# Kernel tuning notes

Measured on AMD Instinct MI355X. Metric: run time of the kernel, lower is better.

Reference implementation:

```python
import jax, jax.numpy as jnp
import numpy as np

PRE, POST, BATCH, HIST = 2048, 2048, 64, 50
CONN_PROB = 0.1


def setup_inputs() -> dict:
    key = jax.random.key(0)
    k1, k2, k3, k4 = jax.random.split(key, 4)
    pre_spikes = jax.random.uniform(k1, (BATCH, PRE), dtype=jnp.float32)
    post_spikes = jax.random.uniform(k2, (BATCH, POST), dtype=jnp.float32)
    connectivity_mask = (jax.random.uniform(k3, (PRE, POST)) < CONN_PROB).astype(jnp.float32)
    synaptic_weights = jax.random.normal(k4, (PRE, POST), dtype=jnp.float32) * 0.1 * connectivity_mask
    return {
        "pre_spikes": pre_spikes,
        "post_spikes": post_spikes,
        "current_time": 0,  # <= 1.0 -> plasticity (formation/pruning) branch skipped, as in warm-up
        "synaptic_weights": synaptic_weights,
        "connectivity_mask": connectivity_mask,
        "pre_activity": jnp.zeros((PRE,), jnp.float32),
        "post_activity": jnp.zeros((POST,), jnp.float32),
        "correlation_history": jnp.zeros((PRE, POST, HIST), jnp.float32),
        "connection_lifetimes": jnp.zeros((PRE, POST), jnp.float32),
        "correlation_index": 7,  # static rolling-buffer write position
    }


def reference(pre_spikes, post_spikes, current_time, synaptic_weights,
              connectivity_mask, pre_activity, post_activity,
              correlation_history, connection_lifetimes, correlation_index):
    # EMA activity traces
    pre_mean = pre_spikes.mean(axis=0)    # [PRE]
    post_mean = post_spikes.mean(axis=0)  # [POST]
    new_pre_activity = 0.99 * pre_activity + 0.01 * pre_mean
    new_post_activity = 0.99 * post_activity + 0.01 * post_mean

    # scatter outer-product correlation into rolling history buffer
    idx = correlation_index % HIST
    current_correlation = jnp.outer(pre_mean, post_mean)              # [PRE, POST]
    new_history = correlation_history.at[:, :, idx].set(current_correlation)

    # masked weight matmul
    effective_weights = synaptic_weights * connectivity_mask          # [PRE, POST]
    synaptic_current = pre_spikes @ effective_weights                 # [BATCH, POST]

    # connection lifetime accumulation
    new_lifetimes = connection_lifetimes + connectivity_mask

    avg_correlation = new_history.mean(axis=-1)                       # [PRE, POST]
    return (synaptic_current, new_pre_activity, new_post_activity,
            new_history, new_lifetimes, avg_correlation)
```

## Files before the change

### kernel.cpp

```cpp
#include <hip/hip_runtime.h>

#define PRE   2048
#define POST  2048
#define BATCH 64
#define HIST  50

#define OFF_SYN      0
#define OFF_PRE_ACT  131072
#define OFF_POST_ACT 133120
#define OFF_HIST     135168
#define OFF_LIFE     209850368
#define OFF_AVG      214044672

__global__ __launch_bounds__(256) void k_means(
    const float* __restrict__ pre, const float* __restrict__ post,
    const float* __restrict__ pre_act, const float* __restrict__ post_act,
    float* __restrict__ out, float* __restrict__ ws_means) {
  const int t = blockIdx.x * 256 + threadIdx.x;

  float4* outz = reinterpret_cast<float4*>(out + OFF_SYN);
  const float4 z = make_float4(0.f, 0.f, 0.f, 0.f);
#pragma unroll
  for (int i = 0; i < 8; ++i) outz[t + i * 4096] = z;

  if (t < PRE) {
    float s = 0.f;
#pragma unroll 8
    for (int b = 0; b < BATCH; ++b) s += pre[b * PRE + t];
    const float m = s * (1.0f / BATCH);
    ws_means[t] = m;
    out[OFF_PRE_ACT + t] = 0.99f * pre_act[t] + 0.01f * m;
  } else {
    const int c = t - PRE;
    float s = 0.f;
#pragma unroll 8
    for (int b = 0; b < BATCH; ++b) s += post[b * POST + c];
    const float m = s * (1.0f / BATCH);
    ws_means[PRE + c] = m;
    out[OFF_POST_ACT + c] = 0.99f * post_act[c] + 0.01f * m;
  }
}

__global__ __launch_bounds__(256) void k_matmul(
    const float* __restrict__ pre, const float* __restrict__ W,
    const float* __restrict__ M, float* __restrict__ out) {
  __shared__ float ew[64 * 256];

  const int jt = blockIdx.x & 7;
  const int ks = blockIdx.x >> 3;
  const int j0 = jt * 256;
  const int k0 = ks * 64;
  const int t = threadIdx.x;

#pragma unroll
  for (int it = 0; it < 16; ++it) {
    const int lin = (t + it * 256) * 4;
    const int kk = lin >> 8;
    const int jj = lin & 255;
    const float4 w4 = *reinterpret_cast<const float4*>(&W[(k0 + kk) * POST + j0 + jj]);
    const float4 m4 = *reinterpret_cast<const float4*>(&M[(k0 + kk) * POST + j0 + jj]);
    float4 e;
    e.x = w4.x * m4.x; e.y = w4.y * m4.y; e.z = w4.z * m4.z; e.w = w4.w * m4.w;
    *reinterpret_cast<float4*>(&ew[kk * 256 + jj]) = e;
  }
  __syncthreads();

  const int tj = t & 31;
  const int tb = t >> 5;
  const int jb = tj * 8;
  const int bb0 = tb * 8;

  float acc[8][8];
#pragma unroll
  for (int r = 0; r < 8; ++r)
#pragma unroll
    for (int c = 0; c < 8; ++c) acc[r][c] = 0.f;

  const float4* ew4 = reinterpret_cast<const float4*>(ew);

  for (int kk4 = 0; kk4 < 16; ++kk4) {
    float4 pr[8];
#pragma unroll
    for (int r = 0; r < 8; ++r)
      pr[r] = *reinterpret_cast<const float4*>(&pre[(bb0 + r) * PRE + k0 + kk4 * 4]);
#pragma unroll
    for (int e = 0; e < 4; ++e) {
      const int kk = kk4 * 4 + e;
      const float4 e0 = ew4[kk * 64 + tj * 2];
      const float4 e1 = ew4[kk * 64 + tj * 2 + 1];
#pragma unroll
      for (int r = 0; r < 8; ++r) {
        const float pv = (e == 0) ? pr[r].x : (e == 1) ? pr[r].y : (e == 2) ? pr[r].z : pr[r].w;
        acc[r][0] += pv * e0.x; acc[r][1] += pv * e0.y;
        acc[r][2] += pv * e0.z; acc[r][3] += pv * e0.w;
        acc[r][4] += pv * e1.x; acc[r][5] += pv * e1.y;
        acc[r][6] += pv * e1.z; acc[r][7] += pv * e1.w;
      }
    }
  }

#pragma unroll
  for (int r = 0; r < 8; ++r)
#pragma unroll
    for (int c = 0; c < 8; ++c)
      unsafeAtomicAdd(&out[OFF_SYN + (bb0 + r) * POST + j0 + jb + c], acc[r][c]);
}

__global__ __launch_bounds__(256) void k_history(
    const float* __restrict__ hist_in, const float* __restrict__ mask,
    const float* __restrict__ life_in, const float* __restrict__ ws_means,
    const int* __restrict__ corr_idx, float* __restrict__ out) {
  __shared__ float lds[256 * 51];

  const int t = threadIdx.x;
  const int pair0 = blockIdx.x * 256;
  const int i_row = pair0 >> 11;
  const int jbase = pair0 & 2047;

  int idx = corr_idx[0] % HIST;
  if (idx < 0) idx += HIST;

  const float mp_i = ws_means[i_row];
  const float* __restrict__ hsrc = hist_in + (size_t)pair0 * HIST;
  float* __restrict__ hdst = out + OFF_HIST + (size_t)pair0 * HIST;
  const float* __restrict__ mpost = ws_means + PRE + jbase;

  for (int v = t; v < 3200; v += 256) {
    const int f = v * 4;
    float4 x = *reinterpret_cast<const float4*>(&hsrc[f]);
    float vals[4] = {x.x, x.y, x.z, x.w};
#pragma unroll
    for (int e = 0; e < 4; ++e) {
      const int ff = f + e;
      const int p = ff / 50;
      const int h = ff - p * 50;
      float val = vals[e];
      if (h == idx) val = mp_i * mpost[p];
      lds[p * 51 + h] = val;
      vals[e] = val;
    }
    x.x = vals[0]; x.y = vals[1]; x.z = vals[2]; x.w = vals[3];
    *reinterpret_cast<float4*>(&hdst[f]) = x;
  }
  __syncthreads();

  float s = 0.f;
#pragma unroll
  for (int h = 0; h < HIST; ++h) s += lds[t * 51 + h];
  const size_t pg = (size_t)pair0 + t;
  out[OFF_AVG + pg] = s * (1.0f / HIST);
  out[OFF_LIFE + pg] = life_in[pg] + mask[pg];
}

extern "C" void kernel_launch(void* const* d_in, const int* in_sizes, int n_in,
                              void* d_out, int out_size, void* d_ws, size_t ws_size,
                              hipStream_t stream) {
  const float* pre   = (const float*)d_in[0];
  const float* post  = (const float*)d_in[1];
  const float* W     = (const float*)d_in[3];
  const float* Mask  = (const float*)d_in[4];
  const float* preA  = (const float*)d_in[5];
  const float* postA = (const float*)d_in[6];
  const float* hist  = (const float*)d_in[7];
  const float* life  = (const float*)d_in[8];
  const int*   cidx  = (const int*)d_in[9];
  float* out = (float*)d_out;
  float* means = (float*)d_ws;

  k_means<<<16, 256, 0, stream>>>(pre, post, preA, postA, out, means);
  k_matmul<<<256, 256, 0, stream>>>(pre, W, Mask, out);
  k_history<<<16384, 256, 0, stream>>>(hist, Mask, life, means, cidx, out);
}
```

Measured before the change: 1.718 ms.

## Use nontemporal vector copies in history kernel and retile matmul

The history kernel now uses 320 threads so each thread copies exactly 10 float4 chunks, with nontemporal loads and stores, and writes whole float4s to unpadded LDS. The per-element divide is replaced by one divide per chunk plus a wrap check. The 50-float row sum reads the LDS with float2 loads. The matmul is retiled to 128-column tiles with a 4x8 accumulator per thread and 512 blocks, and the means loop is unrolled further. The unpadded LDS stride of 50 may cause bank conflicts in the reduction, and the extra 64 threads are idle during the reduction.

```diff
diff --git a/kernel.cpp b/kernel.cpp
--- a/kernel.cpp
+++ b/kernel.cpp
@@ -12,20 +12,22 @@
 #define OFF_LIFE     209850368
 #define OFF_AVG      214044672
 
+typedef float f32x4 __attribute__((ext_vector_type(4)));
+
 __global__ __launch_bounds__(256) void k_means(
     const float* __restrict__ pre, const float* __restrict__ post,
     const float* __restrict__ pre_act, const float* __restrict__ post_act,
     float* __restrict__ out, float* __restrict__ ws_means) {
   const int t = blockIdx.x * 256 + threadIdx.x;
 
-  float4* outz = reinterpret_cast<float4*>(out + OFF_SYN);
-  const float4 z = make_float4(0.f, 0.f, 0.f, 0.f);
+  f32x4* outz = reinterpret_cast<f32x4*>(out + OFF_SYN);
+  const f32x4 z = {0.f, 0.f, 0.f, 0.f};
 #pragma unroll
   for (int i = 0; i < 8; ++i) outz[t + i * 4096] = z;
 
   if (t < PRE) {
     float s = 0.f;
-#pragma unroll 8
+#pragma unroll 16
     for (int b = 0; b < BATCH; ++b) s += pre[b * PRE + t];
     const float m = s * (1.0f / BATCH);
     ws_means[t] = m;
@@ -33,7 +35,7 @@
   } else {
     const int c = t - PRE;
     float s = 0.f;
-#pragma unroll 8
+#pragma unroll 16
     for (int b = 0; b < BATCH; ++b) s += post[b * POST + c];
     const float m = s * (1.0f / BATCH);
     ws_means[PRE + c] = m;
@@ -44,52 +46,53 @@
 __global__ __launch_bounds__(256) void k_matmul(
     const float* __restrict__ pre, const float* __restrict__ W,
     const float* __restrict__ M, float* __restrict__ out) {
-  __shared__ float ew[64 * 256];
+  __shared__ float ew[64 * 128];
 
-  const int jt = blockIdx.x & 7;
-  const int ks = blockIdx.x >> 3;
-  const int j0 = jt * 256;
+  const int jt = blockIdx.x & 15;
+  const int ks = blockIdx.x >> 4;
+  const int j0 = jt * 128;
   const int k0 = ks * 64;
   const int t = threadIdx.x;
 
 #pragma unroll
-  for (int it = 0; it < 16; ++it) {
+  for (int it = 0; it < 8; ++it) {
     const int lin = (t + it * 256) * 4;
-    const int kk = lin >> 8;
-    const int jj = lin & 255;
+    const int kk = lin >> 7;
+    const int jj = lin & 127;
     const float4 w4 = *reinterpret_cast<const float4*>(&W[(k0 + kk) * POST + j0 + jj]);
     const float4 m4 = *reinterpret_cast<const float4*>(&M[(k0 + kk) * POST + j0 + jj]);
     float4 e;
     e.x = w4.x * m4.x; e.y = w4.y * m4.y; e.z = w4.z * m4.z; e.w = w4.w * m4.w;
-    *reinterpret_cast<float4*>(&ew[kk * 256 + jj]) = e;
+    *reinterpret_cast<float4*>(&ew[kk * 128 + jj]) = e;
   }
   __syncthreads();
 
-  const int tj = t & 31;
-  const int tb = t >> 5;
+  const int tj = t & 15;
+  const int tb = t >> 4;
   const int jb = tj * 8;
-  const int bb0 = tb * 8;
+  const int bb0 = tb * 4;
 
-  float acc[8][8];
+  float acc[4][8];
 #pragma unroll
-  for (int r = 0; r < 8; ++r)
+  for (int r = 0; r < 4; ++r)
 #pragma unroll
     for (int c = 0; c < 8; ++c) acc[r][c] = 0.f;
 
   const float4* ew4 = reinterpret_cast<const float4*>(ew);
 
+#pragma unroll
   for (int kk4 = 0; kk4 < 16; ++kk4) {
-    float4 pr[8];
+    float4 pr[4];
 #pragma unroll
-    for (int r = 0; r < 8; ++r)
+    for (int r = 0; r < 4; ++r)
       pr[r] = *reinterpret_cast<const float4*>(&pre[(bb0 + r) * PRE + k0 + kk4 * 4]);
 #pragma unroll
     for (int e = 0; e < 4; ++e) {
       const int kk = kk4 * 4 + e;
-      const float4 e0 = ew4[kk * 64 + tj * 2];
-      const float4 e1 = ew4[kk * 64 + tj * 2 + 1];
+      const float4 e0 = ew4[kk * 32 + tj * 2];
+      const float4 e1 = ew4[kk * 32 + tj * 2 + 1];
 #pragma unroll
-      for (int r = 0; r < 8; ++r) {
+      for (int r = 0; r < 4; ++r) {
         const float pv = (e == 0) ? pr[r].x : (e == 1) ? pr[r].y : (e == 2) ? pr[r].z : pr[r].w;
         acc[r][0] += pv * e0.x; acc[r][1] += pv * e0.y;
         acc[r][2] += pv * e0.z; acc[r][3] += pv * e0.w;
@@ -100,17 +103,17 @@
   }
 
 #pragma unroll
-  for (int r = 0; r < 8; ++r)
+  for (int r = 0; r < 4; ++r)
 #pragma unroll
     for (int c = 0; c < 8; ++c)
       unsafeAtomicAdd(&out[OFF_SYN + (bb0 + r) * POST + j0 + jb + c], acc[r][c]);
 }
 
-__global__ __launch_bounds__(256) void k_history(
+__global__ __launch_bounds__(320) void k_history(
     const float* __restrict__ hist_in, const float* __restrict__ mask,
     const float* __restrict__ life_in, const float* __restrict__ ws_means,
     const int* __restrict__ corr_idx, float* __restrict__ out) {
-  __shared__ float lds[256 * 51];
+  __shared__ float lds[256 * HIST];
 
   const int t = threadIdx.x;
   const int pair0 = blockIdx.x * 256;
@@ -125,31 +128,41 @@
   float* __restrict__ hdst = out + OFF_HIST + (size_t)pair0 * HIST;
   const float* __restrict__ mpost = ws_means + PRE + jbase;
 
-  for (int v = t; v < 3200; v += 256) {
+  const f32x4* __restrict__ hsrc4 = reinterpret_cast<const f32x4*>(hsrc);
+  f32x4* __restrict__ hdst4 = reinterpret_cast<f32x4*>(hdst);
+  f32x4* __restrict__ lds4 = reinterpret_cast<f32x4*>(lds);
+
+#pragma unroll
+  for (int it = 0; it < 10; ++it) {
+    const int v = t + it * 320;
     const int f = v * 4;
-    float4 x = *reinterpret_cast<const float4*>(&hsrc[f]);
-    float vals[4] = {x.x, x.y, x.z, x.w};
+    f32x4 x = __builtin_nontemporal_load(&hsrc4[v]);
+    const int p0 = f / 50;
+    const int h0 = f - p0 * 50;
 #pragma unroll
     for (int e = 0; e < 4; ++e) {
-      const int ff = f + e;
-      const int p = ff / 50;
-      const int h = ff - p * 50;
-      float val = vals[e];
-      if (h == idx) val = mp_i * mpost[p];
-      lds[p * 51 + h] = val;
-      vals[e] = val;
+      int h = h0 + e;
+      int p = p0;
+      if (h >= 50) { h -= 50; ++p; }
+      if (h == idx) x[e] = mp_i * mpost[p];
     }
-    x.x = vals[0]; x.y = vals[1]; x.z = vals[2]; x.w = vals[3];
-    *reinterpret_cast<float4*>(&hdst[f]) = x;
+    lds4[v] = x;
+    __builtin_nontemporal_store(x, &hdst4[v]);
   }
   __syncthreads();
 
-  float s = 0.f;
+  if (t < 256) {
+    const float2* __restrict__ l2 = reinterpret_cast<const float2*>(lds);
+    float s = 0.f;
 #pragma unroll
-  for (int h = 0; h < HIST; ++h) s += lds[t * 51 + h];
-  const size_t pg = (size_t)pair0 + t;
-  out[OFF_AVG + pg] = s * (1.0f / HIST);
-  out[OFF_LIFE + pg] = life_in[pg] + mask[pg];
+    for (int u = 0; u < 25; ++u) {
+      const float2 y = l2[t * 25 + u];
+      s += y.x + y.y;
+    }
+    const size_t pg = (size_t)pair0 + t;
+    out[OFF_AVG + pg] = s * (1.0f / HIST);
+    out[OFF_LIFE + pg] = life_in[pg] + mask[pg];
+  }
 }
 
 extern "C" void kernel_launch(void* const* d_in, const int* in_sizes, int n_in,
@@ -168,6 +181,6 @@
   float* means = (float*)d_ws;
 
   k_means<<<16, 256, 0, stream>>>(pre, post, preA, postA, out, means);
-  k_matmul<<<256, 256, 0, stream>>>(pre, W, Mask, out);
-  k_history<<<16384, 256, 0, stream>>>(hist, Mask, life, means, cidx, out);
+  k_matmul<<<512, 256, 0, stream>>>(pre, W, Mask, out);
+  k_history<<<16384, 320, 0, stream>>>(hist, Mask, life, means, cidx, out);
 }
```

Result: no change. 1.752 ms (+2.0%).
